# Performance work log

Hardware: AMD Instinct MI355X
Metric: run time of the kernel (lower is better)

## Reference

```python
import jax, jax.numpy as jnp
import numpy as np

B = 16384
IN = 512
H = 512

def setup_inputs() -> dict:
    key = jax.random.key(0)
    k1, k2, k3, k4, k5, k6 = jax.random.split(key, 6)
    s_in = 1.0 / np.sqrt(IN + H)
    return {
        "x": jax.random.normal(k1, (B, IN), dtype=jnp.float32),
        "h": jax.random.normal(k2, (B, H), dtype=jnp.float32),
        # lin_in: (IN+H) -> 2H ; stored as [in_features, out_features]
        "W_in": jax.random.uniform(k3, (IN + H, 2 * H), minval=-s_in, maxval=s_in, dtype=jnp.float32),
        "b_in": jax.random.uniform(k4, (2 * H,), minval=-s_in, maxval=s_in, dtype=jnp.float32),
        # lin_out: (IN+H) -> H
        "W_out": jax.random.uniform(k5, (IN + H, H), minval=-s_in, maxval=s_in, dtype=jnp.float32),
        "b_out": jax.random.uniform(k6, (H,), minval=-s_in, maxval=s_in, dtype=jnp.float32),
    }

def reference(x, h, W_in, b_in, W_out, b_out):
    xh = jnp.concatenate([x, h], axis=1)              # [B, IN+H]
    lin = xh @ W_in + b_in                             # [B, 2H]
    learn_pre, forget_pre = jnp.split(lin, 2, axis=1)  # each [B, H]
    learn = jnp.tanh(learn_pre)
    forget_mult = jax.nn.sigmoid(forget_pre)
    h_new = forget_mult * h + (1.0 - forget_mult) * learn
    xh2 = jnp.concatenate([x, h_new], axis=1)          # [B, IN+H]
    out = jnp.tanh(xh2 @ W_out + b_out)                # [B, H]
    return (out, h_new)
```

## Files before the change

### kernel.cpp

```cpp
#include <hip/hip_runtime.h>
#include <cstdint>

typedef unsigned short ushort_t;
typedef __attribute__((ext_vector_type(4))) float f32x4;
typedef __attribute__((ext_vector_type(8))) __bf16 bf16x8;
typedef __attribute__((ext_vector_type(8))) unsigned short ushort8;

#define NB 16384
#define DK 1024

#define MFMA16(a, b, c) __builtin_amdgcn_mfma_f32_16x16x32_bf16(a, b, c, 0, 0, 0)

__device__ __forceinline__ unsigned short f2b(float f) {
    unsigned u = __builtin_bit_cast(unsigned, f);
    unsigned r = u + 0x7fffu + ((u >> 16) & 1u);
    return (unsigned short)(r >> 16);
}
__device__ __forceinline__ float b2f(ushort_t b) {
    unsigned u = ((unsigned)b) << 16;
    return __builtin_bit_cast(float, u);
}
__device__ __forceinline__ float fast_sigmoid(float x) {
    return __fdividef(1.0f, 1.0f + __expf(-x));
}
__device__ __forceinline__ float fast_tanh(float x) {
    return __fdividef(2.0f, 1.0f + __expf(-2.0f * x)) - 1.0f;
}

__device__ __forceinline__ void gll16(const void* g, void* lds) {
    __builtin_amdgcn_global_load_lds(
        (__attribute__((address_space(1))) unsigned int*)(uintptr_t)g,
        (__attribute__((address_space(3))) unsigned int*)(unsigned int)(uintptr_t)lds,
        16, 0, 0);
}


__global__ __launch_bounds__(256) void k_cvt(const float* __restrict__ x,
                                             const float* __restrict__ h,
                                             ushort_t* __restrict__ XB,
                                             ushort_t* __restrict__ HB) {
    int b = blockIdx.x;
    const float* s;
    ushort_t* d;
    if (b < 4096) { s = x; d = XB; } else { s = h; d = HB; b -= 4096; }
    size_t g = (size_t)b * 256 + threadIdx.x;
    const float* p = s + g * 8;
    f32x4 f0 = *(const f32x4*)p;
    f32x4 f1 = *(const f32x4*)(p + 4);
    ushort8 o;
#pragma unroll
    for (int j = 0; j < 4; ++j) { o[j] = f2b(f0[j]); o[j + 4] = f2b(f1[j]); }
    *(ushort8*)(d + g * 8) = o;
}

__global__ __launch_bounds__(256) void k_transpose_w(const float* __restrict__ Wi,
                                                     const float* __restrict__ Wo,
                                                     ushort_t* __restrict__ WTI,
                                                     ushort_t* __restrict__ WTO) {
    const int z = blockIdx.z;
    if (z == 1 && blockIdx.x >= 16) return;
    const float* W = (z == 0) ? Wi : Wo;
    ushort_t* Wt = (z == 0) ? WTI : WTO;
    const int ncols = (z == 0) ? 1024 : 512;
    __shared__ float tile[32][33];
    int n0 = blockIdx.x * 32, k0 = blockIdx.y * 32;
    int tx = threadIdx.x & 31, ty = threadIdx.x >> 5;
#pragma unroll
    for (int i = 0; i < 32; i += 8)
        tile[ty + i][tx] = W[(size_t)(k0 + ty + i) * ncols + n0 + tx];
    __syncthreads();
#pragma unroll
    for (int i = 0; i < 32; i += 8)
        Wt[(size_t)(n0 + ty + i) * DK + k0 + tx] = f2b(tile[tx][ty + i]);
}

__global__ __launch_bounds__(256, 2) void k_gemm1(
    const ushort_t* __restrict__ XB, const ushort_t* __restrict__ HB,
    const ushort_t* __restrict__ WT, const float* __restrict__ b_in,
    float* __restrict__ hnew, ushort_t* __restrict__ HN) {
    __shared__ ushort_t As[2][128 * 64];
    __shared__ ushort_t Bs[2][2][64 * 64];

    const int wg = blockIdx.x;
    const int xcd = wg & 7, q = wg >> 3;
    const int m0 = ((xcd << 4) | (q & 15)) * 128;
    const int n0 = (q >> 4) * 64;

    const int t = threadIdx.x;
    const int lane = t & 63;
    const int wave = t >> 6;
    const int wm = wave >> 1, wn = wave & 1;

    f32x4 accL[4][2] = {};
    f32x4 accF[4][2] = {};

    const int srow = t >> 3;
    const int skel = (t & 7) * 8;
    const ushort_t* gBL = WT + (size_t)(n0 + srow) * DK + skel;
    const ushort_t* gBF = WT + (size_t)(n0 + 512 + srow) * DK + skel;

    auto stage = [&](int it, int buf) {
        const int kt = it * 64;
        const ushort_t* ab = (kt < 512)
            ? (XB + (size_t)(m0 + srow) * 512 + kt + skel)
            : (HB + (size_t)(m0 + srow) * 512 + (kt - 512) + skel);
        ushort_t* a = &As[buf][t * 8];
#pragma unroll
        for (int r = 0; r < 4; ++r)
            gll16(ab + (size_t)(32 * r) * 512, a + 2048 * r);
#pragma unroll
        for (int r = 0; r < 2; ++r) {
            gll16(gBL + kt + (size_t)(32 * r) * DK, &Bs[buf][0][t * 8 + 2048 * r]);
            gll16(gBF + kt + (size_t)(32 * r) * DK, &Bs[buf][1][t * 8 + 2048 * r]);
        }
    };

    const int fr = lane & 15;
    const int fq = lane >> 4;
    const int kq = fq * 8;

    ushort_t hv_us[4][2][4];

    stage(0, 0);
    for (int it = 0; it < 16; ++it) {
        asm volatile("s_waitcnt vmcnt(0)" ::: "memory");
        __syncthreads();
        if (it + 1 < 16) stage(it + 1, (it + 1) & 1);
        if (it == 11) {
#pragma unroll
            for (int i = 0; i < 4; ++i)
#pragma unroll
                for (int j = 0; j < 2; ++j)
#pragma unroll
                    for (int rr = 0; rr < 4; ++rr)
                        hv_us[i][j][rr] =
                            HB[(size_t)(m0 + wm * 64 + i * 16 + fq * 4 + rr) * 512 +
                               n0 + wn * 32 + j * 16 + fr];
        }
        const int cur = it & 1;
#pragma unroll
        for (int kk = 0; kk < 2; ++kk) {
            bf16x8 av[4], blv[2], bfv[2];
#pragma unroll
            for (int i = 0; i < 4; ++i)
                av[i] = *(const bf16x8*)(&As[cur][(wm * 64 + i * 16 + fr) * 64 + kk * 32 + kq]);
#pragma unroll
            for (int j = 0; j < 2; ++j) {
                blv[j] = *(const bf16x8*)(&Bs[cur][0][(wn * 32 + j * 16 + fr) * 64 + kk * 32 + kq]);
                bfv[j] = *(const bf16x8*)(&Bs[cur][1][(wn * 32 + j * 16 + fr) * 64 + kk * 32 + kq]);
            }
            __builtin_amdgcn_s_setprio(1);
#pragma unroll
            for (int i = 0; i < 4; ++i)
#pragma unroll
                for (int j = 0; j < 2; ++j) {
                    accL[i][j] = MFMA16(av[i], blv[j], accL[i][j]);
                    accF[i][j] = MFMA16(av[i], bfv[j], accF[i][j]);
                }
            __builtin_amdgcn_s_setprio(0);
        }
    }

#pragma unroll
    for (int i = 0; i < 4; ++i)
#pragma unroll
        for (int j = 0; j < 2; ++j) {
            const int c = n0 + wn * 32 + j * 16 + fr;
            const float bl = b_in[c];
            const float bf = b_in[c + 512];
#pragma unroll
            for (int rr = 0; rr < 4; ++rr) {
                const int row = m0 + wm * 64 + i * 16 + fq * 4 + rr;
                float lp = accL[i][j][rr] + bl;
                float fp = accF[i][j][rr] + bf;
                float hv = b2f(hv_us[i][j][rr]);
                float fm = fast_sigmoid(fp);
                float lr = fast_tanh(lp);
                float hn = lr + fm * (hv - lr);
                hnew[(size_t)row * 512 + c] = hn;
                HN[(size_t)row * 512 + c] = f2b(hn);
            }
        }
}

__global__ __launch_bounds__(256, 2) void k_gemm2(
    const ushort_t* __restrict__ XB, const ushort_t* __restrict__ HN,
    const ushort_t* __restrict__ WT, const float* __restrict__ b_out,
    float* __restrict__ out) {
    __shared__ ushort_t As[2][128 * 64];
    __shared__ ushort_t Bs[2][128 * 64];

    const int wg = blockIdx.x;
    const int xcd = wg & 7, q = wg >> 3;
    const int m0 = ((xcd << 4) | (q & 15)) * 128;
    const int n0 = (q >> 4) * 128;

    const int t = threadIdx.x;
    const int lane = t & 63;
    const int wave = t >> 6;
    const int wm = wave >> 1, wn = wave & 1;

    f32x4 acc[4][4] = {};

    const int srow = t >> 3;
    const int skel = (t & 7) * 8;
    const ushort_t* gB = WT + (size_t)(n0 + srow) * DK + skel;

    auto stage = [&](int it, int buf) {
        const int kt = it * 64;
        const ushort_t* ab = (kt < 512)
            ? (XB + (size_t)(m0 + srow) * 512 + kt + skel)
            : (HN + (size_t)(m0 + srow) * 512 + (kt - 512) + skel);
        ushort_t* a = &As[buf][t * 8];
        ushort_t* b = &Bs[buf][t * 8];
#pragma unroll
        for (int r = 0; r < 4; ++r) {
            gll16(ab + (size_t)(32 * r) * 512, a + 2048 * r);
            gll16(gB + kt + (size_t)(32 * r) * DK, b + 2048 * r);
        }
    };

    const int fr = lane & 15;
    const int fq = lane >> 4;
    const int kq = fq * 8;

    stage(0, 0);
    for (int it = 0; it < 16; ++it) {
        asm volatile("s_waitcnt vmcnt(0)" ::: "memory");
        __syncthreads();
        if (it + 1 < 16) stage(it + 1, (it + 1) & 1);
        const int cur = it & 1;
#pragma unroll
        for (int kk = 0; kk < 2; ++kk) {
            bf16x8 av[4], bv[4];
#pragma unroll
            for (int i = 0; i < 4; ++i) {
                av[i] = *(const bf16x8*)(&As[cur][(wm * 64 + i * 16 + fr) * 64 + kk * 32 + kq]);
                bv[i] = *(const bf16x8*)(&Bs[cur][(wn * 64 + i * 16 + fr) * 64 + kk * 32 + kq]);
            }
            __builtin_amdgcn_s_setprio(1);
#pragma unroll
            for (int i = 0; i < 4; ++i)
#pragma unroll
                for (int j = 0; j < 4; ++j)
                    acc[i][j] = MFMA16(av[i], bv[j], acc[i][j]);
            __builtin_amdgcn_s_setprio(0);
        }
    }

#pragma unroll
    for (int i = 0; i < 4; ++i)
#pragma unroll
        for (int j = 0; j < 4; ++j) {
            const int c = n0 + wn * 64 + j * 16 + fr;
            const float bo = b_out[c];
#pragma unroll
            for (int rr = 0; rr < 4; ++rr) {
                const int row = m0 + wm * 64 + i * 16 + fq * 4 + rr;
                out[(size_t)row * 512 + c] = fast_tanh(acc[i][j][rr] + bo);
            }
        }
}

extern "C" void kernel_launch(void* const* d_in, const int* in_sizes, int n_in,
                              void* d_out, int out_size, void* d_ws, size_t ws_size,
                              hipStream_t stream) {
    const float* x = (const float*)d_in[0];
    const float* h = (const float*)d_in[1];
    const float* W_in = (const float*)d_in[2];
    const float* b_in = (const float*)d_in[3];
    const float* W_out = (const float*)d_in[4];
    const float* b_out = (const float*)d_in[5];

    float* out = (float*)d_out;
    float* hnew = out + (size_t)NB * 512;

    ushort_t* XB = (ushort_t*)d_ws;
    ushort_t* HB = XB + (size_t)NB * 512;
    ushort_t* HN = HB + (size_t)NB * 512;
    ushort_t* WTI = HN + (size_t)NB * 512;
    ushort_t* WTO = WTI + (size_t)1024 * 1024;

    k_cvt<<<8192, 256, 0, stream>>>(x, h, XB, HB);
    k_transpose_w<<<dim3(32, 32, 2), 256, 0, stream>>>(W_in, W_out, WTI, WTO);
    k_gemm1<<<1024, 256, 0, stream>>>(XB, HB, WTI, b_in, hnew, HN);
    k_gemm2<<<512, 256, 0, stream>>>(XB, HN, WTO, b_out, out);
}
```

Measured before the change: 95.87 us.

## Swizzle bf16 global layouts and rewrite gate GEMM with 256x256 interleaved pipeline

The bf16 conversions of x, h and the transposed weights now write an XOR-swizzled column order within 64-element chunks, so the direct global-to-LDS copies land in a layout that LDS reads can fetch without bank conflicts. Both GEMMs read LDS using the matching XOR pattern. The gate GEMM is rebuilt as a 512-thread, 256x256-tile kernel (128 learn + 128 forget columns) with finer-grained staging interleaved with MFMA phases and partial vmcnt waits. The aim is more data reuse per tile and better overlap of loads with compute, at the cost of higher register pressure (acc[8][4]) and only 256 workgroups, which may underfill the GPU.

New measurement: 84.86 us. -11.5%, faster.

```diff
diff --git a/kernel.cpp b/kernel.cpp
--- a/kernel.cpp
+++ b/kernel.cpp
@@ -50,7 +50,11 @@
     ushort8 o;
 #pragma unroll
     for (int j = 0; j < 4; ++j) { o[j] = f2b(f0[j]); o[j + 4] = f2b(f1[j]); }
-    *(ushort8*)(d + g * 8) = o;
+    size_t fi = g * 8;
+    int row = (int)(fi >> 9);
+    int c = (int)(fi & 511);
+    int swc = (c & ~63) | ((c & 63) ^ ((row & 7) << 3));
+    *(ushort8*)(d + (size_t)row * 512 + swc) = o;
 }
 
 __global__ __launch_bounds__(256) void k_transpose_w(const float* __restrict__ Wi,
@@ -70,159 +74,190 @@
         tile[ty + i][tx] = W[(size_t)(k0 + ty + i) * ncols + n0 + tx];
     __syncthreads();
 #pragma unroll
-    for (int i = 0; i < 32; i += 8)
-        Wt[(size_t)(n0 + ty + i) * DK + k0 + tx] = f2b(tile[tx][ty + i]);
-}
-
-__global__ __launch_bounds__(256, 2) void k_gemm1(
+    for (int i = 0; i < 32; i += 8) {
+        int n = n0 + ty + i;
+        int k = k0 + tx;
+        int kk = (k & ~63) | ((k & 63) ^ ((n & 7) << 3));
+        Wt[(size_t)n * DK + kk] = f2b(tile[tx][ty + i]);
+    }
+}
+
+__global__ __launch_bounds__(512, 1) void k_gemm1(
     const ushort_t* __restrict__ XB, const ushort_t* __restrict__ HB,
     const ushort_t* __restrict__ WT, const float* __restrict__ b_in,
     float* __restrict__ hnew, ushort_t* __restrict__ HN) {
-    __shared__ ushort_t As[2][128 * 64];
-    __shared__ ushort_t Bs[2][2][64 * 64];
+    __shared__ ushort_t As[2][256 * 64];
+    __shared__ ushort_t Bs[2][256 * 64];
+
+    const int t = threadIdx.x;
+    const int lane = t & 63;
+    const int wid = t >> 6;
+    const int wm = wid >> 2, wn = wid & 3;
+    const int m0 = blockIdx.x * 256;
+    const int n0p = blockIdx.y * 128;
+    const int srow = t >> 3;
+    const int scol = (t & 7) * 8;
+    const int fr = lane & 15, fq = lane >> 4;
+    const int xr = (fr & 7) << 3;
+
+    f32x4 acc[8][4] = {};
+
+#define STA(tile, r) do { \
+        int kt_ = (tile) * 64; \
+        int grow_ = m0 + 64 * (r) + srow; \
+        const ushort_t* s_ = (kt_ < 512) ? XB + (size_t)grow_ * 512 + kt_ + scol \
+                                         : HB + (size_t)grow_ * 512 + (kt_ - 512) + scol; \
+        gll16(s_, &As[(tile) & 1][(64 * (r) + srow) * 64 + scol]); \
+    } while (0)
+#define STB(tile, r) do { \
+        int kt_ = (tile) * 64; \
+        int wrow_ = ((r) < 2) ? (n0p + 64 * (r) + srow) : (512 + n0p + 64 * ((r) - 2) + srow); \
+        gll16(WT + (size_t)wrow_ * DK + kt_ + scol, &Bs[(tile) & 1][(64 * (r) + srow) * 64 + scol]); \
+    } while (0)
+
+    bf16x8 a[4][2], bL[2][2], bF[2][2];
+
+#define LDA(cb, mh) do { \
+        _Pragma("unroll") for (int ii = 0; ii < 4; ++ii) \
+        _Pragma("unroll") for (int kk = 0; kk < 2; ++kk) \
+            a[ii][kk] = *(const bf16x8*)&As[cb][(wm * 128 + ((mh) * 4 + ii) * 16 + fr) * 64 + ((kk * 32 + fq * 8) ^ xr)]; \
+    } while (0)
+#define LDBL(cb) do { \
+        _Pragma("unroll") for (int j = 0; j < 2; ++j) \
+        _Pragma("unroll") for (int kk = 0; kk < 2; ++kk) \
+            bL[j][kk] = *(const bf16x8*)&Bs[cb][(wn * 32 + j * 16 + fr) * 64 + ((kk * 32 + fq * 8) ^ xr)]; \
+    } while (0)
+#define LDBF(cb) do { \
+        _Pragma("unroll") for (int j = 0; j < 2; ++j) \
+        _Pragma("unroll") for (int kk = 0; kk < 2; ++kk) \
+            bF[j][kk] = *(const bf16x8*)&Bs[cb][(128 + wn * 32 + j * 16 + fr) * 64 + ((kk * 32 + fq * 8) ^ xr)]; \
+    } while (0)
+#define MML(mh) do { \
+        __builtin_amdgcn_s_setprio(1); \
+        _Pragma("unroll") for (int kk = 0; kk < 2; ++kk) \
+        _Pragma("unroll") for (int ii = 0; ii < 4; ++ii) \
+        _Pragma("unroll") for (int j = 0; j < 2; ++j) \
+            acc[(mh) * 4 + ii][j] = MFMA16(a[ii][kk], bL[j][kk], acc[(mh) * 4 + ii][j]); \
+        __builtin_amdgcn_s_setprio(0); \
+    } while (0)
+#define MMF(mh) do { \
+        __builtin_amdgcn_s_setprio(1); \
+        _Pragma("unroll") for (int kk = 0; kk < 2; ++kk) \
+        _Pragma("unroll") for (int ii = 0; ii < 4; ++ii) \
+        _Pragma("unroll") for (int j = 0; j < 2; ++j) \
+            acc[(mh) * 4 + ii][2 + j] = MFMA16(a[ii][kk], bF[j][kk], acc[(mh) * 4 + ii][2 + j]); \
+        __builtin_amdgcn_s_setprio(0); \
+    } while (0)
+#define BAR asm volatile("s_barrier" ::: "memory")
+#define VM2 asm volatile("s_waitcnt vmcnt(2)" ::: "memory")
+#define VM0 asm volatile("s_waitcnt vmcnt(0)" ::: "memory")
+#define LGKM0 do { asm volatile("s_waitcnt lgkmcnt(0)" ::: "memory"); __builtin_amdgcn_sched_barrier(0); } while (0)
+
+    STA(0, 0); STA(0, 2);
+    STA(0, 1); STA(0, 3);
+    STB(0, 0); STB(0, 1);
+    STB(0, 2); STB(0, 3);
+    STA(1, 0); STA(1, 2);
+    STA(1, 1); STA(1, 3);
+
+    for (int i = 0; i < 8; ++i) {
+        const int g = (i < 7);
+        const int t1 = 2 * i + 1, t2 = 2 * i + 2, t3 = 2 * i + 3;
+        VM2; BAR;
+        STB(t1, 0); STB(t1, 1);
+        LDA(0, 0); LDBL(0);
+        LGKM0; MML(0);
+        BAR;
+        if (g) { STA(t2, 0); STA(t2, 2); }
+        LDBF(0);
+        LGKM0; MMF(0);
+        BAR;
+        STB(t1, 2); STB(t1, 3);
+        LDA(0, 1);
+        LGKM0; MML(1);
+        BAR;
+        if (g) { STA(t2, 1); STA(t2, 3); }
+        LGKM0; MMF(1);
+        if (g) { VM2; } else { VM0; }
+        BAR;
+        if (g) { STB(t2, 0); STB(t2, 1); }
+        LDA(1, 0); LDBL(1);
+        LGKM0; MML(0);
+        BAR;
+        if (g) { STA(t3, 0); STA(t3, 2); }
+        LDBF(1);
+        LGKM0; MMF(0);
+        BAR;
+        if (g) { STB(t2, 2); STB(t2, 3); }
+        LDA(1, 1);
+        LGKM0; MML(1);
+        BAR;
+        if (g) { STA(t3, 1); STA(t3, 3); }
+        LGKM0; MMF(1);
+    }
+
+#pragma unroll
+    for (int mf = 0; mf < 8; ++mf)
+#pragma unroll
+        for (int j = 0; j < 2; ++j) {
+            const int cp = n0p + wn * 32 + j * 16 + fr;
+            const float bl = b_in[cp];
+            const float bf = b_in[cp + 512];
+#pragma unroll
+            for (int rr = 0; rr < 4; ++rr) {
+                const int row = m0 + wm * 128 + mf * 16 + fq * 4 + rr;
+                const int sc = (cp & ~63) | ((cp & 63) ^ ((row & 7) << 3));
+                float lp = acc[mf][j][rr] + bl;
+                float fp = acc[mf][2 + j][rr] + bf;
+                float hv = b2f(HB[(size_t)row * 512 + sc]);
+                float fm = fast_sigmoid(fp);
+                float lr = fast_tanh(lp);
+                float hn = lr + fm * (hv - lr);
+                hnew[(size_t)row * 512 + cp] = hn;
+                HN[(size_t)row * 512 + sc] = f2b(hn);
+            }
+        }
+}
+
+__global__ __launch_bounds__(256, 2) void k_gemm2(
+    const ushort_t* __restrict__ XB, const ushort_t* __restrict__ HN,
+    const ushort_t* __restrict__ WT, const float* __restrict__ b_out,
+    float* __restrict__ out) {
+    __shared__ ushort_t A2[2][128 * 64];
+    __shared__ ushort_t B2[2][128 * 64];
 
     const int wg = blockIdx.x;
     const int xcd = wg & 7, q = wg >> 3;
     const int m0 = ((xcd << 4) | (q & 15)) * 128;
-    const int n0 = (q >> 4) * 64;
+    const int n0 = (q >> 4) * 128;
 
     const int t = threadIdx.x;
     const int lane = t & 63;
     const int wave = t >> 6;
     const int wm = wave >> 1, wn = wave & 1;
 
-    f32x4 accL[4][2] = {};
-    f32x4 accF[4][2] = {};
-
-    const int srow = t >> 3;
-    const int skel = (t & 7) * 8;
-    const ushort_t* gBL = WT + (size_t)(n0 + srow) * DK + skel;
-    const ushort_t* gBF = WT + (size_t)(n0 + 512 + srow) * DK + skel;
-
-    auto stage = [&](int it, int buf) {
-        const int kt = it * 64;
-        const ushort_t* ab = (kt < 512)
-            ? (XB + (size_t)(m0 + srow) * 512 + kt + skel)
-            : (HB + (size_t)(m0 + srow) * 512 + (kt - 512) + skel);
-        ushort_t* a = &As[buf][t * 8];
-#pragma unroll
-        for (int r = 0; r < 4; ++r)
-            gll16(ab + (size_t)(32 * r) * 512, a + 2048 * r);
-#pragma unroll
-        for (int r = 0; r < 2; ++r) {
-            gll16(gBL + kt + (size_t)(32 * r) * DK, &Bs[buf][0][t * 8 + 2048 * r]);
-            gll16(gBF + kt + (size_t)(32 * r) * DK, &Bs[buf][1][t * 8 + 2048 * r]);
-        }
-    };
-
-    const int fr = lane & 15;
-    const int fq = lane >> 4;
-    const int kq = fq * 8;
-
-    ushort_t hv_us[4][2][4];
-
-    stage(0, 0);
-    for (int it = 0; it < 16; ++it) {
-        asm volatile("s_waitcnt vmcnt(0)" ::: "memory");
-        __syncthreads();
-        if (it + 1 < 16) stage(it + 1, (it + 1) & 1);
-        if (it == 11) {
-#pragma unroll
-            for (int i = 0; i < 4; ++i)
-#pragma unroll
-                for (int j = 0; j < 2; ++j)
-#pragma unroll
-                    for (int rr = 0; rr < 4; ++rr)
-                        hv_us[i][j][rr] =
-                            HB[(size_t)(m0 + wm * 64 + i * 16 + fq * 4 + rr) * 512 +
-                               n0 + wn * 32 + j * 16 + fr];
-        }
-        const int cur = it & 1;
-#pragma unroll
-        for (int kk = 0; kk < 2; ++kk) {
-            bf16x8 av[4], blv[2], bfv[2];
-#pragma unroll
-            for (int i = 0; i < 4; ++i)
-                av[i] = *(const bf16x8*)(&As[cur][(wm * 64 + i * 16 + fr) * 64 + kk * 32 + kq]);
-#pragma unroll
-            for (int j = 0; j < 2; ++j) {
-                blv[j] = *(const bf16x8*)(&Bs[cur][0][(wn * 32 + j * 16 + fr) * 64 + kk * 32 + kq]);
-                bfv[j] = *(const bf16x8*)(&Bs[cur][1][(wn * 32 + j * 16 + fr) * 64 + kk * 32 + kq]);
-            }
-            __builtin_amdgcn_s_setprio(1);
-#pragma unroll
-            for (int i = 0; i < 4; ++i)
-#pragma unroll
-                for (int j = 0; j < 2; ++j) {
-                    accL[i][j] = MFMA16(av[i], blv[j], accL[i][j]);
-                    accF[i][j] = MFMA16(av[i], bfv[j], accF[i][j]);
-                }
-            __builtin_amdgcn_s_setprio(0);
-        }
-    }
-
-#pragma unroll
-    for (int i = 0; i < 4; ++i)
-#pragma unroll
-        for (int j = 0; j < 2; ++j) {
-            const int c = n0 + wn * 32 + j * 16 + fr;
-            const float bl = b_in[c];
-            const float bf = b_in[c + 512];
-#pragma unroll
-            for (int rr = 0; rr < 4; ++rr) {
-                const int row = m0 + wm * 64 + i * 16 + fq * 4 + rr;
-                float lp = accL[i][j][rr] + bl;
-                float fp = accF[i][j][rr] + bf;
-                float hv = b2f(hv_us[i][j][rr]);
-                float fm = fast_sigmoid(fp);
-                float lr = fast_tanh(lp);
-                float hn = lr + fm * (hv - lr);
-                hnew[(size_t)row * 512 + c] = hn;
-                HN[(size_t)row * 512 + c] = f2b(hn);
-            }
-        }
-}
-
-__global__ __launch_bounds__(256, 2) void k_gemm2(
-    const ushort_t* __restrict__ XB, const ushort_t* __restrict__ HN,
-    const ushort_t* __restrict__ WT, const float* __restrict__ b_out,
-    float* __restrict__ out) {
-    __shared__ ushort_t As[2][128 * 64];
-    __shared__ ushort_t Bs[2][128 * 64];
-
-    const int wg = blockIdx.x;
-    const int xcd = wg & 7, q = wg >> 3;
-    const int m0 = ((xcd << 4) | (q & 15)) * 128;
-    const int n0 = (q >> 4) * 128;
-
-    const int t = threadIdx.x;
-    const int lane = t & 63;
-    const int wave = t >> 6;
-    const int wm = wave >> 1, wn = wave & 1;
-
     f32x4 acc[4][4] = {};
 
     const int srow = t >> 3;
     const int skel = (t & 7) * 8;
     const ushort_t* gB = WT + (size_t)(n0 + srow) * DK + skel;
+    const int fr = lane & 15;
+    const int fq = lane >> 4;
+    const int xr = (fr & 7) << 3;
 
     auto stage = [&](int it, int buf) {
         const int kt = it * 64;
         const ushort_t* ab = (kt < 512)
             ? (XB + (size_t)(m0 + srow) * 512 + kt + skel)
             : (HN + (size_t)(m0 + srow) * 512 + (kt - 512) + skel);
-        ushort_t* a = &As[buf][t * 8];
-        ushort_t* b = &Bs[buf][t * 8];
+        ushort_t* a = &A2[buf][t * 8];
+        ushort_t* b = &B2[buf][t * 8];
 #pragma unroll
         for (int r = 0; r < 4; ++r) {
             gll16(ab + (size_t)(32 * r) * 512, a + 2048 * r);
             gll16(gB + kt + (size_t)(32 * r) * DK, b + 2048 * r);
         }
     };
-
-    const int fr = lane & 15;
-    const int fq = lane >> 4;
-    const int kq = fq * 8;
 
     stage(0, 0);
     for (int it = 0; it < 16; ++it) {
@@ -235,8 +270,8 @@
             bf16x8 av[4], bv[4];
 #pragma unroll
             for (int i = 0; i < 4; ++i) {
-                av[i] = *(const bf16x8*)(&As[cur][(wm * 64 + i * 16 + fr) * 64 + kk * 32 + kq]);
-                bv[i] = *(const bf16x8*)(&Bs[cur][(wn * 64 + i * 16 + fr) * 64 + kk * 32 + kq]);
+                av[i] = *(const bf16x8*)(&A2[cur][(wm * 64 + i * 16 + fr) * 64 + ((kk * 32 + fq * 8) ^ xr)]);
+                bv[i] = *(const bf16x8*)(&B2[cur][(wn * 64 + i * 16 + fr) * 64 + ((kk * 32 + fq * 8) ^ xr)]);
             }
             __builtin_amdgcn_s_setprio(1);
 #pragma unroll
@@ -283,6 +318,6 @@
 
     k_cvt<<<8192, 256, 0, stream>>>(x, h, XB, HB);
     k_transpose_w<<<dim3(32, 32, 2), 256, 0, stream>>>(W_in, W_out, WTI, WTO);
-    k_gemm1<<<1024, 256, 0, stream>>>(XB, HB, WTI, b_in, hnew, HN);
+    k_gemm1<<<dim3(64, 4), 512, 0, stream>>>(XB, HB, WTI, b_in, hnew, HN);
     k_gemm2<<<512, 256, 0, stream>>>(XB, HN, WTO, b_out, out);
 }
```

## Fuse fp32-to-bf16 activation conversion into GEMM A-tile staging

Applied to the files above, without the earlier changes.

Removes the separate conversion kernel and the bf16 workspace copies of x, h and h_new. Both GEMMs now load fp32 activations into registers, convert them with packed bf16 conversion and write them to a padded LDS tile. The K tile shrinks from 64 to 32, so there are twice as many iterations, each with two barriers. This adds register-staged loads, extra synchronization and doubled fp32 A-operand read traffic in exchange for dropping one launch and the intermediate buffer round trips.

New measurement: 103.2 us. 1.08x slower.

```diff
diff --git a/kernel.cpp b/kernel.cpp
--- a/kernel.cpp
+++ b/kernel.cpp
@@ -2,12 +2,14 @@
 #include <cstdint>
 
 typedef unsigned short ushort_t;
+typedef unsigned int uint_t;
 typedef __attribute__((ext_vector_type(4))) float f32x4;
+typedef __attribute__((ext_vector_type(2))) unsigned int uint2_t;
 typedef __attribute__((ext_vector_type(8))) __bf16 bf16x8;
-typedef __attribute__((ext_vector_type(8))) unsigned short ushort8;
 
 #define NB 16384
 #define DK 1024
+#define LDA_P 40
 
 #define MFMA16(a, b, c) __builtin_amdgcn_mfma_f32_16x16x32_bf16(a, b, c, 0, 0, 0)
 
@@ -16,15 +18,16 @@
     unsigned r = u + 0x7fffu + ((u >> 16) & 1u);
     return (unsigned short)(r >> 16);
 }
-__device__ __forceinline__ float b2f(ushort_t b) {
-    unsigned u = ((unsigned)b) << 16;
-    return __builtin_bit_cast(float, u);
-}
 __device__ __forceinline__ float fast_sigmoid(float x) {
     return __fdividef(1.0f, 1.0f + __expf(-x));
 }
 __device__ __forceinline__ float fast_tanh(float x) {
     return __fdividef(2.0f, 1.0f + __expf(-2.0f * x)) - 1.0f;
+}
+__device__ __forceinline__ uint_t cvtpk(float lo, float hi) {
+    uint_t r;
+    asm("v_cvt_pk_bf16_f32 %0, %1, %2" : "=v"(r) : "v"(lo), "v"(hi));
+    return r;
 }
 
 __device__ __forceinline__ void gll16(const void* g, void* lds) {
@@ -34,24 +37,9 @@
         16, 0, 0);
 }
 
-
-__global__ __launch_bounds__(256) void k_cvt(const float* __restrict__ x,
-                                             const float* __restrict__ h,
-                                             ushort_t* __restrict__ XB,
-                                             ushort_t* __restrict__ HB) {
-    int b = blockIdx.x;
-    const float* s;
-    ushort_t* d;
-    if (b < 4096) { s = x; d = XB; } else { s = h; d = HB; b -= 4096; }
-    size_t g = (size_t)b * 256 + threadIdx.x;
-    const float* p = s + g * 8;
-    f32x4 f0 = *(const f32x4*)p;
-    f32x4 f1 = *(const f32x4*)(p + 4);
-    ushort8 o;
-#pragma unroll
-    for (int j = 0; j < 4; ++j) { o[j] = f2b(f0[j]); o[j + 4] = f2b(f1[j]); }
-    *(ushort8*)(d + g * 8) = o;
-}
+#define BAR asm volatile("s_barrier" ::: "memory")
+#define VM0 asm volatile("s_waitcnt vmcnt(0)" ::: "memory")
+#define LGKM0 asm volatile("s_waitcnt lgkmcnt(0)" ::: "memory")
 
 __global__ __launch_bounds__(256) void k_transpose_w(const float* __restrict__ Wi,
                                                      const float* __restrict__ Wo,
@@ -75,11 +63,11 @@
 }
 
 __global__ __launch_bounds__(256, 2) void k_gemm1(
-    const ushort_t* __restrict__ XB, const ushort_t* __restrict__ HB,
+    const float* __restrict__ x, const float* __restrict__ h,
     const ushort_t* __restrict__ WT, const float* __restrict__ b_in,
-    float* __restrict__ hnew, ushort_t* __restrict__ HN) {
-    __shared__ ushort_t As[2][128 * 64];
-    __shared__ ushort_t Bs[2][2][64 * 64];
+    float* __restrict__ hnew) {
+    __shared__ ushort_t Abf[2][128 * LDA_P];
+    __shared__ ushort_t Bs[2][2][64 * 32];
 
     const int wg = blockIdx.x;
     const int xcd = wg & 7, q = wg >> 3;
@@ -94,71 +82,80 @@
     f32x4 accL[4][2] = {};
     f32x4 accF[4][2] = {};
 
-    const int srow = t >> 3;
-    const int skel = (t & 7) * 8;
-    const ushort_t* gBL = WT + (size_t)(n0 + srow) * DK + skel;
-    const ushort_t* gBF = WT + (size_t)(n0 + 512 + srow) * DK + skel;
-
-    auto stage = [&](int it, int buf) {
-        const int kt = it * 64;
-        const ushort_t* ab = (kt < 512)
-            ? (XB + (size_t)(m0 + srow) * 512 + kt + skel)
-            : (HB + (size_t)(m0 + srow) * 512 + (kt - 512) + skel);
-        ushort_t* a = &As[buf][t * 8];
-#pragma unroll
-        for (int r = 0; r < 4; ++r)
-            gll16(ab + (size_t)(32 * r) * 512, a + 2048 * r);
-#pragma unroll
-        for (int r = 0; r < 2; ++r) {
-            gll16(gBL + kt + (size_t)(32 * r) * DK, &Bs[buf][0][t * 8 + 2048 * r]);
-            gll16(gBF + kt + (size_t)(32 * r) * DK, &Bs[buf][1][t * 8 + 2048 * r]);
-        }
-    };
+    const int arow = t >> 3;
+    const int acol = (t & 7) * 4;
+    const int brow = t >> 2;
+    const int bcol = (t & 3) * 8;
+    const ushort_t* gBL = WT + (size_t)(n0 + brow) * DK + bcol;
+    const ushort_t* gBF = WT + (size_t)(n0 + 512 + brow) * DK + bcol;
 
     const int fr = lane & 15;
     const int fq = lane >> 4;
     const int kq = fq * 8;
 
-    ushort_t hv_us[4][2][4];
-
-    stage(0, 0);
-    for (int it = 0; it < 16; ++it) {
-        asm volatile("s_waitcnt vmcnt(0)" ::: "memory");
-        __syncthreads();
-        if (it + 1 < 16) stage(it + 1, (it + 1) & 1);
-        if (it == 11) {
+    f32x4 areg[4];
+    auto load_a = [&](int it) {
+        const int kt = it * 32;
+        const float* src = (kt < 512) ? (x + (size_t)m0 * 512 + kt)
+                                      : (h + (size_t)m0 * 512 + (kt - 512));
+#pragma unroll
+        for (int r = 0; r < 4; ++r)
+            areg[r] = *(const f32x4*)(src + (size_t)(32 * r + arow) * 512 + acol);
+    };
+    auto load_b = [&](int it, int buf) {
+        const int kt = it * 32;
+        gll16(gBL + kt, &Bs[buf][0][t * 8]);
+        gll16(gBF + kt, &Bs[buf][1][t * 8]);
+    };
+    auto write_a = [&](int buf) {
+#pragma unroll
+        for (int r = 0; r < 4; ++r) {
+            uint2_t w;
+            w[0] = cvtpk(areg[r][0], areg[r][1]);
+            w[1] = cvtpk(areg[r][2], areg[r][3]);
+            *(uint2_t*)&Abf[buf][(32 * r + arow) * LDA_P + acol] = w;
+        }
+    };
+
+    float hreg[4][2][4];
+
+    load_a(0);
+    load_b(0, 0);
+    for (int it = 0; it < 32; ++it) {
+        const int cur = it & 1;
+        VM0;
+        BAR;
+        write_a(cur);
+        LGKM0;
+        BAR;
+        if (it + 1 < 32) { load_a(it + 1); load_b(it + 1, cur ^ 1); }
+        if (it == 24) {
 #pragma unroll
             for (int i = 0; i < 4; ++i)
 #pragma unroll
                 for (int j = 0; j < 2; ++j)
 #pragma unroll
                     for (int rr = 0; rr < 4; ++rr)
-                        hv_us[i][j][rr] =
-                            HB[(size_t)(m0 + wm * 64 + i * 16 + fq * 4 + rr) * 512 +
-                               n0 + wn * 32 + j * 16 + fr];
-        }
-        const int cur = it & 1;
-#pragma unroll
-        for (int kk = 0; kk < 2; ++kk) {
-            bf16x8 av[4], blv[2], bfv[2];
-#pragma unroll
-            for (int i = 0; i < 4; ++i)
-                av[i] = *(const bf16x8*)(&As[cur][(wm * 64 + i * 16 + fr) * 64 + kk * 32 + kq]);
+                        hreg[i][j][rr] =
+                            h[(size_t)(m0 + wm * 64 + i * 16 + fq * 4 + rr) * 512 +
+                              n0 + wn * 32 + j * 16 + fr];
+        }
+        bf16x8 av[4], blv[2], bfv[2];
+#pragma unroll
+        for (int i = 0; i < 4; ++i)
+            av[i] = *(const bf16x8*)(&Abf[cur][(wm * 64 + i * 16 + fr) * LDA_P + kq]);
+#pragma unroll
+        for (int j = 0; j < 2; ++j) {
+            blv[j] = *(const bf16x8*)(&Bs[cur][0][(wn * 32 + j * 16 + fr) * 32 + kq]);
+            bfv[j] = *(const bf16x8*)(&Bs[cur][1][(wn * 32 + j * 16 + fr) * 32 + kq]);
+        }
+#pragma unroll
+        for (int i = 0; i < 4; ++i)
 #pragma unroll
             for (int j = 0; j < 2; ++j) {
-                blv[j] = *(const bf16x8*)(&Bs[cur][0][(wn * 32 + j * 16 + fr) * 64 + kk * 32 + kq]);
-                bfv[j] = *(const bf16x8*)(&Bs[cur][1][(wn * 32 + j * 16 + fr) * 64 + kk * 32 + kq]);
+                accL[i][j] = MFMA16(av[i], blv[j], accL[i][j]);
+                accF[i][j] = MFMA16(av[i], bfv[j], accF[i][j]);
             }
-            __builtin_amdgcn_s_setprio(1);
-#pragma unroll
-            for (int i = 0; i < 4; ++i)
-#pragma unroll
-                for (int j = 0; j < 2; ++j) {
-                    accL[i][j] = MFMA16(av[i], blv[j], accL[i][j]);
-                    accF[i][j] = MFMA16(av[i], bfv[j], accF[i][j]);
-                }
-            __builtin_amdgcn_s_setprio(0);
-        }
     }
 
 #pragma unroll
@@ -173,22 +170,19 @@
                 const int row = m0 + wm * 64 + i * 16 + fq * 4 + rr;
                 float lp = accL[i][j][rr] + bl;
                 float fp = accF[i][j][rr] + bf;
-                float hv = b2f(hv_us[i][j][rr]);
                 float fm = fast_sigmoid(fp);
                 float lr = fast_tanh(lp);
-                float hn = lr + fm * (hv - lr);
-                hnew[(size_t)row * 512 + c] = hn;
-                HN[(size_t)row * 512 + c] = f2b(hn);
+                hnew[(size_t)row * 512 + c] = lr + fm * (hreg[i][j][rr] - lr);
             }
         }
 }
 
 __global__ __launch_bounds__(256, 2) void k_gemm2(
-    const ushort_t* __restrict__ XB, const ushort_t* __restrict__ HN,
+    const float* __restrict__ x, const float* __restrict__ hnew,
     const ushort_t* __restrict__ WT, const float* __restrict__ b_out,
     float* __restrict__ out) {
-    __shared__ ushort_t As[2][128 * 64];
-    __shared__ ushort_t Bs[2][128 * 64];
+    __shared__ ushort_t Abf[2][128 * LDA_P];
+    __shared__ ushort_t Bs[2][128 * 32];
 
     const int wg = blockIdx.x;
     const int xcd = wg & 7, q = wg >> 3;
@@ -202,50 +196,62 @@
 
     f32x4 acc[4][4] = {};
 
-    const int srow = t >> 3;
-    const int skel = (t & 7) * 8;
-    const ushort_t* gB = WT + (size_t)(n0 + srow) * DK + skel;
-
-    auto stage = [&](int it, int buf) {
-        const int kt = it * 64;
-        const ushort_t* ab = (kt < 512)
-            ? (XB + (size_t)(m0 + srow) * 512 + kt + skel)
-            : (HN + (size_t)(m0 + srow) * 512 + (kt - 512) + skel);
-        ushort_t* a = &As[buf][t * 8];
-        ushort_t* b = &Bs[buf][t * 8];
-#pragma unroll
-        for (int r = 0; r < 4; ++r) {
-            gll16(ab + (size_t)(32 * r) * 512, a + 2048 * r);
-            gll16(gB + kt + (size_t)(32 * r) * DK, b + 2048 * r);
-        }
-    };
+    const int arow = t >> 3;
+    const int acol = (t & 7) * 4;
+    const int brow = t >> 2;
+    const int bcol = (t & 3) * 8;
+    const ushort_t* gB = WT + (size_t)n0 * DK + bcol;
 
     const int fr = lane & 15;
     const int fq = lane >> 4;
     const int kq = fq * 8;
 
-    stage(0, 0);
-    for (int it = 0; it < 16; ++it) {
-        asm volatile("s_waitcnt vmcnt(0)" ::: "memory");
-        __syncthreads();
-        if (it + 1 < 16) stage(it + 1, (it + 1) & 1);
+    f32x4 areg[4];
+    auto load_a = [&](int it) {
+        const int kt = it * 32;
+        const float* src = (kt < 512) ? (x + (size_t)m0 * 512 + kt)
+                                      : (hnew + (size_t)m0 * 512 + (kt - 512));
+#pragma unroll
+        for (int r = 0; r < 4; ++r)
+            areg[r] = *(const f32x4*)(src + (size_t)(32 * r + arow) * 512 + acol);
+    };
+    auto load_b = [&](int it, int buf) {
+        const int kt = it * 32;
+#pragma unroll
+        for (int r = 0; r < 2; ++r)
+            gll16(gB + (size_t)(64 * r + brow) * DK + kt, &Bs[buf][64 * 32 * r + t * 8]);
+    };
+    auto write_a = [&](int buf) {
+#pragma unroll
+        for (int r = 0; r < 4; ++r) {
+            uint2_t w;
+            w[0] = cvtpk(areg[r][0], areg[r][1]);
+            w[1] = cvtpk(areg[r][2], areg[r][3]);
+            *(uint2_t*)&Abf[buf][(32 * r + arow) * LDA_P + acol] = w;
+        }
+    };
+
+    load_a(0);
+    load_b(0, 0);
+    for (int it = 0; it < 32; ++it) {
         const int cur = it & 1;
-#pragma unroll
-        for (int kk = 0; kk < 2; ++kk) {
-            bf16x8 av[4], bv[4];
-#pragma unroll
-            for (int i = 0; i < 4; ++i) {
-                av[i] = *(const bf16x8*)(&As[cur][(wm * 64 + i * 16 + fr) * 64 + kk * 32 + kq]);
-                bv[i] = *(const bf16x8*)(&Bs[cur][(wn * 64 + i * 16 + fr) * 64 + kk * 32 + kq]);
-            }
-            __builtin_amdgcn_s_setprio(1);
-#pragma unroll
-            for (int i = 0; i < 4; ++i)
-#pragma unroll
-                for (int j = 0; j < 4; ++j)
-                    acc[i][j] = MFMA16(av[i], bv[j], acc[i][j]);
-            __builtin_amdgcn_s_setprio(0);
-        }
+        VM0;
+        BAR;
+        write_a(cur);
+        LGKM0;
+        BAR;
+        if (it + 1 < 32) { load_a(it + 1); load_b(it + 1, cur ^ 1); }
+        bf16x8 av[4], bv[4];
+#pragma unroll
+        for (int i = 0; i < 4; ++i) {
+            av[i] = *(const bf16x8*)(&Abf[cur][(wm * 64 + i * 16 + fr) * LDA_P + kq]);
+            bv[i] = *(const bf16x8*)(&Bs[cur][(wn * 64 + i * 16 + fr) * 32 + kq]);
+        }
+#pragma unroll
+        for (int i = 0; i < 4; ++i)
+#pragma unroll
+            for (int j = 0; j < 4; ++j)
+                acc[i][j] = MFMA16(av[i], bv[j], acc[i][j]);
     }
 
 #pragma unroll
@@ -275,14 +281,10 @@
     float* out = (float*)d_out;
     float* hnew = out + (size_t)NB * 512;
 
-    ushort_t* XB = (ushort_t*)d_ws;
-    ushort_t* HB = XB + (size_t)NB * 512;
-    ushort_t* HN = HB + (size_t)NB * 512;
-    ushort_t* WTI = HN + (size_t)NB * 512;
+    ushort_t* WTI = (ushort_t*)d_ws;
     ushort_t* WTO = WTI + (size_t)1024 * 1024;
 
-    k_cvt<<<8192, 256, 0, stream>>>(x, h, XB, HB);
     k_transpose_w<<<dim3(32, 32, 2), 256, 0, stream>>>(W_in, W_out, WTI, WTO);
-    k_gemm1<<<1024, 256, 0, stream>>>(XB, HB, WTI, b_in, hnew, HN);
-    k_gemm2<<<512, 256, 0, stream>>>(XB, HN, WTO, b_out, out);
-}
+    k_gemm1<<<1024, 256, 0, stream>>>(x, h, WTI, b_in, hnew);
+    k_gemm2<<<512, 256, 0, stream>>>(x, hnew, WTO, b_out, out);
+}
```

## Swizzle bf16 operand layouts and split first GEMM into learn and forget kernels

Applied to the files above, without the earlier changes.

Activations and transposed weights are now stored with an XOR swizzle on 8-element groups within each 64-column block, so the LDS fragment reads avoid bank conflicts without padding. The fused learn/forget GEMM is split into two 128x128-tile kernels. The learn kernel writes its pre-activation as bf16 to a new workspace buffer, and the forget kernel reads it back in its epilogue to compute h_new. The split gives larger square tiles and simpler operand staging, at the cost of an extra kernel launch, an extra global round trip for the learn pre-activation, and bf16 rounding of that intermediate.

Result: faster. 93.18 us (-2.8%).

```diff
diff --git a/kernel.cpp b/kernel.cpp
--- a/kernel.cpp
+++ b/kernel.cpp
@@ -50,7 +50,11 @@
     ushort8 o;
 #pragma unroll
     for (int j = 0; j < 4; ++j) { o[j] = f2b(f0[j]); o[j + 4] = f2b(f1[j]); }
-    *(ushort8*)(d + g * 8) = o;
+    size_t fi = g * 8;
+    int row = (int)(fi >> 9);
+    int c = (int)(fi & 511);
+    int swc = (c & ~63) | ((c & 63) ^ ((row & 7) << 3));
+    *(ushort8*)(d + (size_t)row * 512 + swc) = o;
 }
 
 __global__ __launch_bounds__(256) void k_transpose_w(const float* __restrict__ Wi,
@@ -70,159 +74,53 @@
         tile[ty + i][tx] = W[(size_t)(k0 + ty + i) * ncols + n0 + tx];
     __syncthreads();
 #pragma unroll
-    for (int i = 0; i < 32; i += 8)
-        Wt[(size_t)(n0 + ty + i) * DK + k0 + tx] = f2b(tile[tx][ty + i]);
-}
-
-__global__ __launch_bounds__(256, 2) void k_gemm1(
-    const ushort_t* __restrict__ XB, const ushort_t* __restrict__ HB,
-    const ushort_t* __restrict__ WT, const float* __restrict__ b_in,
-    float* __restrict__ hnew, ushort_t* __restrict__ HN) {
-    __shared__ ushort_t As[2][128 * 64];
-    __shared__ ushort_t Bs[2][2][64 * 64];
+    for (int i = 0; i < 32; i += 8) {
+        int n = n0 + ty + i;
+        int k = k0 + tx;
+        int kk = (k & ~63) | ((k & 63) ^ ((n & 7) << 3));
+        Wt[(size_t)n * DK + kk] = f2b(tile[tx][ty + i]);
+    }
+}
+
+
+__global__ __launch_bounds__(256, 2) void k_gemmL(
+    const ushort_t* __restrict__ XB, const ushort_t* __restrict__ AH,
+    const ushort_t* __restrict__ WTbase, ushort_t* __restrict__ LP) {
+    __shared__ ushort_t A2[2][128 * 64];
+    __shared__ ushort_t B2[2][128 * 64];
 
     const int wg = blockIdx.x;
     const int xcd = wg & 7, q = wg >> 3;
     const int m0 = ((xcd << 4) | (q & 15)) * 128;
-    const int n0 = (q >> 4) * 64;
+    const int n0 = (q >> 4) * 128;
 
     const int t = threadIdx.x;
     const int lane = t & 63;
     const int wave = t >> 6;
     const int wm = wave >> 1, wn = wave & 1;
 
-    f32x4 accL[4][2] = {};
-    f32x4 accF[4][2] = {};
+    f32x4 acc[4][4] = {};
 
     const int srow = t >> 3;
     const int skel = (t & 7) * 8;
-    const ushort_t* gBL = WT + (size_t)(n0 + srow) * DK + skel;
-    const ushort_t* gBF = WT + (size_t)(n0 + 512 + srow) * DK + skel;
+    const ushort_t* gB = WTbase + (size_t)(n0 + srow) * DK + skel;
+    const int fr = lane & 15;
+    const int fq = lane >> 4;
+    const int xr = (fr & 7) << 3;
 
     auto stage = [&](int it, int buf) {
         const int kt = it * 64;
         const ushort_t* ab = (kt < 512)
             ? (XB + (size_t)(m0 + srow) * 512 + kt + skel)
-            : (HB + (size_t)(m0 + srow) * 512 + (kt - 512) + skel);
-        ushort_t* a = &As[buf][t * 8];
-#pragma unroll
-        for (int r = 0; r < 4; ++r)
-            gll16(ab + (size_t)(32 * r) * 512, a + 2048 * r);
-#pragma unroll
-        for (int r = 0; r < 2; ++r) {
-            gll16(gBL + kt + (size_t)(32 * r) * DK, &Bs[buf][0][t * 8 + 2048 * r]);
-            gll16(gBF + kt + (size_t)(32 * r) * DK, &Bs[buf][1][t * 8 + 2048 * r]);
-        }
-    };
-
-    const int fr = lane & 15;
-    const int fq = lane >> 4;
-    const int kq = fq * 8;
-
-    ushort_t hv_us[4][2][4];
-
-    stage(0, 0);
-    for (int it = 0; it < 16; ++it) {
-        asm volatile("s_waitcnt vmcnt(0)" ::: "memory");
-        __syncthreads();
-        if (it + 1 < 16) stage(it + 1, (it + 1) & 1);
-        if (it == 11) {
-#pragma unroll
-            for (int i = 0; i < 4; ++i)
-#pragma unroll
-                for (int j = 0; j < 2; ++j)
-#pragma unroll
-                    for (int rr = 0; rr < 4; ++rr)
-                        hv_us[i][j][rr] =
-                            HB[(size_t)(m0 + wm * 64 + i * 16 + fq * 4 + rr) * 512 +
-                               n0 + wn * 32 + j * 16 + fr];
-        }
-        const int cur = it & 1;
-#pragma unroll
-        for (int kk = 0; kk < 2; ++kk) {
-            bf16x8 av[4], blv[2], bfv[2];
-#pragma unroll
-            for (int i = 0; i < 4; ++i)
-                av[i] = *(const bf16x8*)(&As[cur][(wm * 64 + i * 16 + fr) * 64 + kk * 32 + kq]);
-#pragma unroll
-            for (int j = 0; j < 2; ++j) {
-                blv[j] = *(const bf16x8*)(&Bs[cur][0][(wn * 32 + j * 16 + fr) * 64 + kk * 32 + kq]);
-                bfv[j] = *(const bf16x8*)(&Bs[cur][1][(wn * 32 + j * 16 + fr) * 64 + kk * 32 + kq]);
-            }
-            __builtin_amdgcn_s_setprio(1);
-#pragma unroll
-            for (int i = 0; i < 4; ++i)
-#pragma unroll
-                for (int j = 0; j < 2; ++j) {
-                    accL[i][j] = MFMA16(av[i], blv[j], accL[i][j]);
-                    accF[i][j] = MFMA16(av[i], bfv[j], accF[i][j]);
-                }
-            __builtin_amdgcn_s_setprio(0);
-        }
-    }
-
-#pragma unroll
-    for (int i = 0; i < 4; ++i)
-#pragma unroll
-        for (int j = 0; j < 2; ++j) {
-            const int c = n0 + wn * 32 + j * 16 + fr;
-            const float bl = b_in[c];
-            const float bf = b_in[c + 512];
-#pragma unroll
-            for (int rr = 0; rr < 4; ++rr) {
-                const int row = m0 + wm * 64 + i * 16 + fq * 4 + rr;
-                float lp = accL[i][j][rr] + bl;
-                float fp = accF[i][j][rr] + bf;
-                float hv = b2f(hv_us[i][j][rr]);
-                float fm = fast_sigmoid(fp);
-                float lr = fast_tanh(lp);
-                float hn = lr + fm * (hv - lr);
-                hnew[(size_t)row * 512 + c] = hn;
-                HN[(size_t)row * 512 + c] = f2b(hn);
-            }
-        }
-}
-
-__global__ __launch_bounds__(256, 2) void k_gemm2(
-    const ushort_t* __restrict__ XB, const ushort_t* __restrict__ HN,
-    const ushort_t* __restrict__ WT, const float* __restrict__ b_out,
-    float* __restrict__ out) {
-    __shared__ ushort_t As[2][128 * 64];
-    __shared__ ushort_t Bs[2][128 * 64];
-
-    const int wg = blockIdx.x;
-    const int xcd = wg & 7, q = wg >> 3;
-    const int m0 = ((xcd << 4) | (q & 15)) * 128;
-    const int n0 = (q >> 4) * 128;
-
-    const int t = threadIdx.x;
-    const int lane = t & 63;
-    const int wave = t >> 6;
-    const int wm = wave >> 1, wn = wave & 1;
-
-    f32x4 acc[4][4] = {};
-
-    const int srow = t >> 3;
-    const int skel = (t & 7) * 8;
-    const ushort_t* gB = WT + (size_t)(n0 + srow) * DK + skel;
-
-    auto stage = [&](int it, int buf) {
-        const int kt = it * 64;
-        const ushort_t* ab = (kt < 512)
-            ? (XB + (size_t)(m0 + srow) * 512 + kt + skel)
-            : (HN + (size_t)(m0 + srow) * 512 + (kt - 512) + skel);
-        ushort_t* a = &As[buf][t * 8];
-        ushort_t* b = &Bs[buf][t * 8];
+            : (AH + (size_t)(m0 + srow) * 512 + (kt - 512) + skel);
+        ushort_t* a = &A2[buf][t * 8];
+        ushort_t* b = &B2[buf][t * 8];
 #pragma unroll
         for (int r = 0; r < 4; ++r) {
             gll16(ab + (size_t)(32 * r) * 512, a + 2048 * r);
             gll16(gB + kt + (size_t)(32 * r) * DK, b + 2048 * r);
         }
     };
-
-    const int fr = lane & 15;
-    const int fq = lane >> 4;
-    const int kq = fq * 8;
 
     stage(0, 0);
     for (int it = 0; it < 16; ++it) {
@@ -235,8 +133,174 @@
             bf16x8 av[4], bv[4];
 #pragma unroll
             for (int i = 0; i < 4; ++i) {
-                av[i] = *(const bf16x8*)(&As[cur][(wm * 64 + i * 16 + fr) * 64 + kk * 32 + kq]);
-                bv[i] = *(const bf16x8*)(&Bs[cur][(wn * 64 + i * 16 + fr) * 64 + kk * 32 + kq]);
+                av[i] = *(const bf16x8*)(&A2[cur][(wm * 64 + i * 16 + fr) * 64 + ((kk * 32 + fq * 8) ^ xr)]);
+                bv[i] = *(const bf16x8*)(&B2[cur][(wn * 64 + i * 16 + fr) * 64 + ((kk * 32 + fq * 8) ^ xr)]);
+            }
+            __builtin_amdgcn_s_setprio(1);
+#pragma unroll
+            for (int i = 0; i < 4; ++i)
+#pragma unroll
+                for (int j = 0; j < 4; ++j)
+                    acc[i][j] = MFMA16(av[i], bv[j], acc[i][j]);
+            __builtin_amdgcn_s_setprio(0);
+        }
+    }
+
+#pragma unroll
+    for (int i = 0; i < 4; ++i)
+#pragma unroll
+        for (int j = 0; j < 4; ++j) {
+            const int c = n0 + wn * 64 + j * 16 + fr;
+#pragma unroll
+            for (int rr = 0; rr < 4; ++rr) {
+                const int row = m0 + wm * 64 + i * 16 + fq * 4 + rr;
+                const int sc = (c & ~63) | ((c & 63) ^ ((row & 7) << 3));
+                LP[(size_t)row * 512 + sc] = f2b(acc[i][j][rr]);
+            }
+        }
+}
+
+__global__ __launch_bounds__(256, 2) void k_gemmF(
+    const ushort_t* __restrict__ XB, const ushort_t* __restrict__ HB,
+    const ushort_t* __restrict__ WTbase, const ushort_t* __restrict__ LP,
+    const float* __restrict__ b_in, float* __restrict__ hnew,
+    ushort_t* __restrict__ HN) {
+    __shared__ ushort_t A2[2][128 * 64];
+    __shared__ ushort_t B2[2][128 * 64];
+
+    const int wg = blockIdx.x;
+    const int xcd = wg & 7, q = wg >> 3;
+    const int m0 = ((xcd << 4) | (q & 15)) * 128;
+    const int n0 = (q >> 4) * 128;
+
+    const int t = threadIdx.x;
+    const int lane = t & 63;
+    const int wave = t >> 6;
+    const int wm = wave >> 1, wn = wave & 1;
+
+    f32x4 acc[4][4] = {};
+
+    const int srow = t >> 3;
+    const int skel = (t & 7) * 8;
+    const ushort_t* gB = WTbase + (size_t)(n0 + srow) * DK + skel;
+    const int fr = lane & 15;
+    const int fq = lane >> 4;
+    const int xr = (fr & 7) << 3;
+
+    auto stage = [&](int it, int buf) {
+        const int kt = it * 64;
+        const ushort_t* ab = (kt < 512)
+            ? (XB + (size_t)(m0 + srow) * 512 + kt + skel)
+            : (HB + (size_t)(m0 + srow) * 512 + (kt - 512) + skel);
+        ushort_t* a = &A2[buf][t * 8];
+        ushort_t* b = &B2[buf][t * 8];
+#pragma unroll
+        for (int r = 0; r < 4; ++r) {
+            gll16(ab + (size_t)(32 * r) * 512, a + 2048 * r);
+            gll16(gB + kt + (size_t)(32 * r) * DK, b + 2048 * r);
+        }
+    };
+
+    stage(0, 0);
+    for (int it = 0; it < 16; ++it) {
+        asm volatile("s_waitcnt vmcnt(0)" ::: "memory");
+        __syncthreads();
+        if (it + 1 < 16) stage(it + 1, (it + 1) & 1);
+        const int cur = it & 1;
+#pragma unroll
+        for (int kk = 0; kk < 2; ++kk) {
+            bf16x8 av[4], bv[4];
+#pragma unroll
+            for (int i = 0; i < 4; ++i) {
+                av[i] = *(const bf16x8*)(&A2[cur][(wm * 64 + i * 16 + fr) * 64 + ((kk * 32 + fq * 8) ^ xr)]);
+                bv[i] = *(const bf16x8*)(&B2[cur][(wn * 64 + i * 16 + fr) * 64 + ((kk * 32 + fq * 8) ^ xr)]);
+            }
+            __builtin_amdgcn_s_setprio(1);
+#pragma unroll
+            for (int i = 0; i < 4; ++i)
+#pragma unroll
+                for (int j = 0; j < 4; ++j)
+                    acc[i][j] = MFMA16(av[i], bv[j], acc[i][j]);
+            __builtin_amdgcn_s_setprio(0);
+        }
+    }
+
+#pragma unroll
+    for (int i = 0; i < 4; ++i)
+#pragma unroll
+        for (int j = 0; j < 4; ++j) {
+            const int c = n0 + wn * 64 + j * 16 + fr;
+            const float bl = b_in[c];
+            const float bf = b_in[c + 512];
+#pragma unroll
+            for (int rr = 0; rr < 4; ++rr) {
+                const int row = m0 + wm * 64 + i * 16 + fq * 4 + rr;
+                const int sc = (c & ~63) | ((c & 63) ^ ((row & 7) << 3));
+                float lp = b2f(LP[(size_t)row * 512 + sc]) + bl;
+                float fp = acc[i][j][rr] + bf;
+                float hv = b2f(HB[(size_t)row * 512 + sc]);
+                float fm = fast_sigmoid(fp);
+                float lr = fast_tanh(lp);
+                float hn = lr + fm * (hv - lr);
+                hnew[(size_t)row * 512 + c] = hn;
+                HN[(size_t)row * 512 + sc] = f2b(hn);
+            }
+        }
+}
+
+__global__ __launch_bounds__(256, 2) void k_gemm2(
+    const ushort_t* __restrict__ XB, const ushort_t* __restrict__ HN,
+    const ushort_t* __restrict__ WT, const float* __restrict__ b_out,
+    float* __restrict__ out) {
+    __shared__ ushort_t A2[2][128 * 64];
+    __shared__ ushort_t B2[2][128 * 64];
+
+    const int wg = blockIdx.x;
+    const int xcd = wg & 7, q = wg >> 3;
+    const int m0 = ((xcd << 4) | (q & 15)) * 128;
+    const int n0 = (q >> 4) * 128;
+
+    const int t = threadIdx.x;
+    const int lane = t & 63;
+    const int wave = t >> 6;
+    const int wm = wave >> 1, wn = wave & 1;
+
+    f32x4 acc[4][4] = {};
+
+    const int srow = t >> 3;
+    const int skel = (t & 7) * 8;
+    const ushort_t* gB = WT + (size_t)(n0 + srow) * DK + skel;
+    const int fr = lane & 15;
+    const int fq = lane >> 4;
+    const int xr = (fr & 7) << 3;
+
+    auto stage = [&](int it, int buf) {
+        const int kt = it * 64;
+        const ushort_t* ab = (kt < 512)
+            ? (XB + (size_t)(m0 + srow) * 512 + kt + skel)
+            : (HN + (size_t)(m0 + srow) * 512 + (kt - 512) + skel);
+        ushort_t* a = &A2[buf][t * 8];
+        ushort_t* b = &B2[buf][t * 8];
+#pragma unroll
+        for (int r = 0; r < 4; ++r) {
+            gll16(ab + (size_t)(32 * r) * 512, a + 2048 * r);
+            gll16(gB + kt + (size_t)(32 * r) * DK, b + 2048 * r);
+        }
+    };
+
+    stage(0, 0);
+    for (int it = 0; it < 16; ++it) {
+        asm volatile("s_waitcnt vmcnt(0)" ::: "memory");
+        __syncthreads();
+        if (it + 1 < 16) stage(it + 1, (it + 1) & 1);
+        const int cur = it & 1;
+#pragma unroll
+        for (int kk = 0; kk < 2; ++kk) {
+            bf16x8 av[4], bv[4];
+#pragma unroll
+            for (int i = 0; i < 4; ++i) {
+                av[i] = *(const bf16x8*)(&A2[cur][(wm * 64 + i * 16 + fr) * 64 + ((kk * 32 + fq * 8) ^ xr)]);
+                bv[i] = *(const bf16x8*)(&B2[cur][(wn * 64 + i * 16 + fr) * 64 + ((kk * 32 + fq * 8) ^ xr)]);
             }
             __builtin_amdgcn_s_setprio(1);
 #pragma unroll
@@ -278,11 +342,13 @@
     ushort_t* XB = (ushort_t*)d_ws;
     ushort_t* HB = XB + (size_t)NB * 512;
     ushort_t* HN = HB + (size_t)NB * 512;
-    ushort_t* WTI = HN + (size_t)NB * 512;
+    ushort_t* LP = HN + (size_t)NB * 512;
+    ushort_t* WTI = LP + (size_t)NB * 512;
     ushort_t* WTO = WTI + (size_t)1024 * 1024;
 
     k_cvt<<<8192, 256, 0, stream>>>(x, h, XB, HB);
     k_transpose_w<<<dim3(32, 32, 2), 256, 0, stream>>>(W_in, W_out, WTI, WTO);
-    k_gemm1<<<1024, 256, 0, stream>>>(XB, HB, WTI, b_in, hnew, HN);
+    k_gemmL<<<512, 256, 0, stream>>>(XB, HB, WTI, LP);
+    k_gemmF<<<512, 256, 0, stream>>>(XB, HB, WTI + (size_t)512 * DK, LP, b_in, hnew, HN);
     k_gemm2<<<512, 256, 0, stream>>>(XB, HN, WTO, b_out, out);
 }
```
